# Optimization experiments

Hardware: AMD Instinct MI355X
Metric: run time of the kernel (lower is better)

The kernel has to match this reference:

```python
import jax, jax.numpy as jnp
import numpy as np

NUM_CAPSULE = 10
DIM_CAPSULE = 16
NUM_ROUTING = 3
EPS = 1e-7  # tf.keras.backend.epsilon()


def squash(v, axis=-1):
    s2 = jnp.sum(jnp.square(v), axis=axis, keepdims=True)
    scale = s2 / (1.0 + s2) / jnp.sqrt(s2 + EPS)
    return scale * v


def setup_inputs() -> dict:
    key = jax.random.key(0)
    k1, k2 = jax.random.split(key)
    B, in_dim = 16384, 2048
    inputs = jax.random.normal(k1, (B, in_dim), dtype=jnp.float32)
    # glorot-uniform-ish scale for the kernel
    limit = np.sqrt(6.0 / (in_dim + NUM_CAPSULE * DIM_CAPSULE)).astype(np.float32)
    kernel = jax.random.uniform(k2, (in_dim, NUM_CAPSULE * DIM_CAPSULE),
                                dtype=jnp.float32, minval=-limit, maxval=limit)
    return {"inputs": inputs, "kernel": kernel}


def reference(inputs, kernel):
    B = inputs.shape[0]
    # [B, in_dim] @ [in_dim, nc*dc] -> [B, nc, dc]
    inputs_hat = (inputs @ kernel).reshape(B, NUM_CAPSULE, DIM_CAPSULE)
    b = jnp.zeros((B, NUM_CAPSULE, 1), dtype=inputs.dtype)
    outputs = None
    for _ in range(NUM_ROUTING):
        c = jax.nn.softmax(b, axis=1)                      # [B, nc, 1]
        s = jnp.sum(c * inputs_hat, axis=1, keepdims=True)  # [B, 1, dc]
        outputs = squash(s)                                 # [B, 1, dc]
        # matmul(inputs_hat, outputs, transpose_b=True) -> [B, nc, 1]
        b = b + jnp.einsum('bnd,bd->bn', inputs_hat, outputs[:, 0, :])[:, :, None]
    return outputs[:, 0, :]  # [B, dc]
```

## Files before the change

### kernel.cpp

```cpp
#include <hip/hip_runtime.h>
#include <hip/hip_bf16.h>

typedef unsigned int u32;
typedef unsigned short u16;
typedef __attribute__((ext_vector_type(8))) __bf16 bf16x8;
typedef __attribute__((ext_vector_type(4))) float f32x4;

#define N_CAP 10
#define D_CAP 16
#define NN 160
#define KK 2048
#define BM 64
#define BK 32
#define NSTEPS (KK / BK)
#define THREADS 640
#define LDST 40
#define AS_TILE (BM * LDST)
#define HAT_STRIDE 164
#define SMEM_BYTES (BM * HAT_STRIDE * 4)

__device__ __forceinline__ u32 pack_hi(float f0, float f1) {
  u32 u0 = __builtin_bit_cast(u32, f0), u1 = __builtin_bit_cast(u32, f1);
  return (u0 >> 16) | (u1 & 0xFFFF0000u);
}
__device__ __forceinline__ float hi_part(float f) {
  u32 u = __builtin_bit_cast(u32, f) & 0xFFFF0000u;
  return __builtin_bit_cast(float, u);
}
union U4B8 { uint4 u; bf16x8 b; };

__global__ __launch_bounds__(THREADS, 3) void capsule_fused(
    const float* __restrict__ X, const float* __restrict__ W, float* __restrict__ out) {
  __shared__ __align__(16) char smem[SMEM_BYTES];
  u16* As_hi = (u16*)smem;
  u16* As_lo = As_hi + AS_TILE;
  float* hat = (float*)smem;

  const int t = threadIdx.x;
  const int rbase = blockIdx.x * BM;
  const int lane = t & 63;
  const int w = t >> 6;
  const int wip = (w >= 5) ? 1 : 0;
  const int wjp = w - 5 * wip;
  const int l15 = lane & 15;
  const int q = lane >> 4;

  const int ar = t >> 2;
  const int ak = (t & 3) * 8;
  const float* gA = X + (size_t)(rbase + ar) * KK + ak;

  const float* gB = W + (q * 8) * NN + 32 * wjp + l15;

  f32x4 acc00 = {0.f,0.f,0.f,0.f}, acc01 = {0.f,0.f,0.f,0.f};
  f32x4 acc10 = {0.f,0.f,0.f,0.f}, acc11 = {0.f,0.f,0.f,0.f};

  float4 pa0A, pa1A, pa0B, pa1B;
  if (t < 256) {
    pa0A = *(const float4*)(gA);            pa1A = *(const float4*)(gA + 4);
    pa0B = *(const float4*)(gA + BK);       pa1B = *(const float4*)(gA + BK + 4);
  }
  float buA[16], buB[16];
#pragma unroll
  for (int j = 0; j < 8; ++j) { buA[j] = gB[j * NN]; buA[8 + j] = gB[16 + j * NN]; }

#define STEP(S, PA0, PA1, BU, BNXT)                                              \
  {                                                                              \
    __syncthreads();                            \
    if (t < 256) {                                                               \
      uint4 hi, lo;                                                              \
      hi.x = pack_hi(PA0.x, PA0.y); hi.y = pack_hi(PA0.z, PA0.w);                \
      hi.z = pack_hi(PA1.x, PA1.y); hi.w = pack_hi(PA1.z, PA1.w);                \
      float l0 = PA0.x - hi_part(PA0.x), l1 = PA0.y - hi_part(PA0.y);            \
      float l2 = PA0.z - hi_part(PA0.z), l3 = PA0.w - hi_part(PA0.w);            \
      float l4 = PA1.x - hi_part(PA1.x), l5 = PA1.y - hi_part(PA1.y);            \
      float l6 = PA1.z - hi_part(PA1.z), l7 = PA1.w - hi_part(PA1.w);            \
      lo.x = pack_hi(l0, l1); lo.y = pack_hi(l2, l3);                            \
      lo.z = pack_hi(l4, l5); lo.w = pack_hi(l6, l7);                            \
      *(uint4*)(As_hi + ar * LDST + ak) = hi;                                    \
      *(uint4*)(As_lo + ar * LDST + ak) = lo;                                    \
    }                                                                            \
    __syncthreads();                                             \
    if (t < 256 && (S) + 2 < NSTEPS) {                                           \
      PA0 = *(const float4*)(gA + ((S) + 2) * BK);                               \
      PA1 = *(const float4*)(gA + ((S) + 2) * BK + 4);                           \
    }                                                                            \
    if ((S) + 1 < NSTEPS) {                                                      \
      const float* b = gB + ((S) + 1) * (BK * NN);                               \
      _Pragma("unroll")                                                          \
      for (int j = 0; j < 8; ++j) { BNXT[j] = b[j * NN]; BNXT[8 + j] = b[16 + j * NN]; } \
    }                                                                            \
    U4B8 bh0, bl0, bh1, bl1;                                                     \
    bh0.u.x = pack_hi(BU[0], BU[1]);  bh0.u.y = pack_hi(BU[2], BU[3]);           \
    bh0.u.z = pack_hi(BU[4], BU[5]);  bh0.u.w = pack_hi(BU[6], BU[7]);           \
    bh1.u.x = pack_hi(BU[8], BU[9]);  bh1.u.y = pack_hi(BU[10], BU[11]);         \
    bh1.u.z = pack_hi(BU[12], BU[13]); bh1.u.w = pack_hi(BU[14], BU[15]);        \
    float lb[16];                                                                \
    _Pragma("unroll")                                                            \
    for (int j = 0; j < 16; ++j) lb[j] = BU[j] - hi_part(BU[j]);                 \
    bl0.u.x = pack_hi(lb[0], lb[1]);  bl0.u.y = pack_hi(lb[2], lb[3]);           \
    bl0.u.z = pack_hi(lb[4], lb[5]);  bl0.u.w = pack_hi(lb[6], lb[7]);           \
    bl1.u.x = pack_hi(lb[8], lb[9]);  bl1.u.y = pack_hi(lb[10], lb[11]);         \
    bl1.u.z = pack_hi(lb[12], lb[13]); bl1.u.w = pack_hi(lb[14], lb[15]);        \
    bf16x8 ah0 = *(const bf16x8*)(As_hi + (32 * wip + l15) * LDST + q * 8);      \
    bf16x8 ah1 = *(const bf16x8*)(As_hi + (32 * wip + 16 + l15) * LDST + q * 8); \
    bf16x8 al0 = *(const bf16x8*)(As_lo + (32 * wip + l15) * LDST + q * 8);      \
    bf16x8 al1 = *(const bf16x8*)(As_lo + (32 * wip + 16 + l15) * LDST + q * 8); \
    acc00 = __builtin_amdgcn_mfma_f32_16x16x32_bf16(ah0, bh0.b, acc00, 0, 0, 0); \
    acc00 = __builtin_amdgcn_mfma_f32_16x16x32_bf16(ah0, bl0.b, acc00, 0, 0, 0); \
    acc00 = __builtin_amdgcn_mfma_f32_16x16x32_bf16(al0, bh0.b, acc00, 0, 0, 0); \
    acc01 = __builtin_amdgcn_mfma_f32_16x16x32_bf16(ah0, bh1.b, acc01, 0, 0, 0); \
    acc01 = __builtin_amdgcn_mfma_f32_16x16x32_bf16(ah0, bl1.b, acc01, 0, 0, 0); \
    acc01 = __builtin_amdgcn_mfma_f32_16x16x32_bf16(al0, bh1.b, acc01, 0, 0, 0); \
    acc10 = __builtin_amdgcn_mfma_f32_16x16x32_bf16(ah1, bh0.b, acc10, 0, 0, 0); \
    acc10 = __builtin_amdgcn_mfma_f32_16x16x32_bf16(ah1, bl0.b, acc10, 0, 0, 0); \
    acc10 = __builtin_amdgcn_mfma_f32_16x16x32_bf16(al1, bh0.b, acc10, 0, 0, 0); \
    acc11 = __builtin_amdgcn_mfma_f32_16x16x32_bf16(ah1, bh1.b, acc11, 0, 0, 0); \
    acc11 = __builtin_amdgcn_mfma_f32_16x16x32_bf16(ah1, bl1.b, acc11, 0, 0, 0); \
    acc11 = __builtin_amdgcn_mfma_f32_16x16x32_bf16(al1, bh1.b, acc11, 0, 0, 0); \
  }

  for (int s = 0; s < NSTEPS; s += 2) {
    STEP(s,     pa0A, pa1A, buA, buB)
    STEP(s + 1, pa0B, pa1B, buB, buA)
  }
#undef STEP

  __syncthreads();
#pragma unroll
  for (int r = 0; r < 4; ++r) {
    const int rowb = 32 * wip + 4 * q + r;
    const int colb = 32 * wjp + l15;
    hat[rowb * HAT_STRIDE + colb]             = acc00[r];
    hat[rowb * HAT_STRIDE + colb + 16]        = acc01[r];
    hat[(rowb + 16) * HAT_STRIDE + colb]      = acc10[r];
    hat[(rowb + 16) * HAT_STRIDE + colb + 16] = acc11[r];
  }
  __syncthreads();

  if (t < BM) {
    const int r = t;
    float bb[N_CAP];
#pragma unroll
    for (int n = 0; n < N_CAP; ++n) bb[n] = 0.f;
    float v[D_CAP];
#pragma unroll
    for (int it = 0; it < 3; ++it) {
      float mx = bb[0];
#pragma unroll
      for (int n = 1; n < N_CAP; ++n) mx = fmaxf(mx, bb[n]);
      float c[N_CAP], se = 0.f;
#pragma unroll
      for (int n = 0; n < N_CAP; ++n) { c[n] = __expf(bb[n] - mx); se += c[n]; }
      const float inv = 1.f / se;
      float sd[D_CAP], s2 = 0.f;
#pragma unroll
      for (int d = 0; d < D_CAP; ++d) {
        float x = 0.f;
#pragma unroll
        for (int n = 0; n < N_CAP; ++n) x += c[n] * hat[r * HAT_STRIDE + n * D_CAP + d];
        x *= inv;
        sd[d] = x;
        s2 += x * x;
      }
      const float scale = s2 / ((1.f + s2) * sqrtf(s2 + 1e-7f));
#pragma unroll
      for (int d = 0; d < D_CAP; ++d) v[d] = scale * sd[d];
      if (it < 2) {
#pragma unroll
        for (int n = 0; n < N_CAP; ++n) {
          float dd = 0.f;
#pragma unroll
          for (int d = 0; d < D_CAP; ++d) dd += hat[r * HAT_STRIDE + n * D_CAP + d] * v[d];
          bb[n] += dd;
        }
      }
    }
#pragma unroll
    for (int d = 0; d < D_CAP; ++d)
      out[(size_t)(rbase + r) * D_CAP + d] = v[d];
  }
}

extern "C" void kernel_launch(void* const* d_in, const int* in_sizes, int n_in,
                              void* d_out, int out_size, void* d_ws, size_t ws_size,
                              hipStream_t stream) {
  const float* X = (const float*)d_in[0];
  const float* W = (const float*)d_in[1];
  if (n_in >= 2 && in_sizes[0] == KK * NN) {
    X = (const float*)d_in[1];
    W = (const float*)d_in[0];
  }
  capsule_fused<<<16384 / BM, THREADS, 0, stream>>>(X, W, (float*)d_out);
}
```

Before: 243.5 us.

## Pre-split weights into bf16 hi/lo fragments and restructure GEMM tiling with double-buffered LDS

Adds a small pre-pass kernel that splits W into bf16 hi and lo parts, stored in an MFMA-fragment-friendly layout in the workspace. The main kernel then loads B fragments directly as bf16x8 vectors instead of doing per-step fp32 loads and conversions. It also moves to 32-row blocks with 320 threads and BK=64, and double-buffers the A tile in LDS so there is one barrier per step instead of two. The cost is an extra kernel launch and a pass over W each call, plus more, smaller blocks. The old kernel is kept as a fallback when the workspace is too small.

```diff
diff --git a/kernel.cpp b/kernel.cpp
--- a/kernel.cpp
+++ b/kernel.cpp
@@ -10,6 +10,197 @@
 #define D_CAP 16
 #define NN 160
 #define KK 2048
+
+__device__ __forceinline__ u32 pack_hi(float f0, float f1) {
+  u32 u0 = __builtin_bit_cast(u32, f0), u1 = __builtin_bit_cast(u32, f1);
+  return (u0 >> 16) | (u1 & 0xFFFF0000u);
+}
+__device__ __forceinline__ float hi_part(float f) {
+  u32 u = __builtin_bit_cast(u32, f) & 0xFFFF0000u;
+  return __builtin_bit_cast(float, u);
+}
+union U4B8 { uint4 u; bf16x8 b; };
+
+__global__ void split_w(const float* __restrict__ W, u16* __restrict__ Whi,
+                        u16* __restrict__ Wlo) {
+  const int tid = blockIdx.x * 256 + threadIdx.x;
+  const int k = tid / NN, n = tid - k * NN;
+  const float f = W[tid];
+  const u32 u = __builtin_bit_cast(u32, f);
+  const float lo = f - hi_part(f);
+  const int dst = ((k >> 3) * NN + n) * 8 + (k & 7);
+  Whi[dst] = (u16)(u >> 16);
+  Wlo[dst] = (u16)(__builtin_bit_cast(u32, lo) >> 16);
+}
+
+#define BM2 32
+#define BK2 64
+#define NST2 (KK / BK2)
+#define THR2 320
+#define LDST2 72
+#define ATILE2 2304
+#define BUFU16 4608
+#define SMEM2 20992
+
+__global__ __launch_bounds__(THR2, 3) void capsule_main(
+    const float* __restrict__ X, const u16* __restrict__ Whi,
+    const u16* __restrict__ Wlo, float* __restrict__ out) {
+  __shared__ __align__(16) char smem[SMEM2];
+  u16* As = (u16*)smem;
+  float* hat = (float*)smem;
+
+  const int t = threadIdx.x;
+  const int rbase = blockIdx.x * BM2;
+  const int lane = t & 63;
+  const int w = t >> 6;
+  const int l15 = lane & 15;
+  const int q = lane >> 4;
+
+  const int ar = t >> 3;
+  const int ak = (t & 7) * 8;
+  const float* gA = X + (size_t)(rbase + ar) * KK + ak;
+  const int wA = ar * LDST2 + ak;
+
+  const int gB0 = (q * NN + 32 * w + l15) * 8;
+
+  f32x4 acc00 = {0,0,0,0}, acc01 = {0,0,0,0}, acc10 = {0,0,0,0}, acc11 = {0,0,0,0};
+
+  float4 paA0, paA1, paB0, paB1;
+  bf16x8 BAh[2][2], BAl[2][2], BBh[2][2], BBl[2][2];
+
+  if (t < 256) {
+    paA0 = *(const float4*)(gA);            paA1 = *(const float4*)(gA + 4);
+    paB0 = *(const float4*)(gA + BK2);      paB1 = *(const float4*)(gA + BK2 + 4);
+  }
+#pragma unroll
+  for (int h = 0; h < 2; ++h)
+#pragma unroll
+    for (int i = 0; i < 2; ++i) {
+      BAh[h][i] = *(const bf16x8*)(Whi + gB0 + h * 5120 + i * 128);
+      BAl[h][i] = *(const bf16x8*)(Wlo + gB0 + h * 5120 + i * 128);
+    }
+  if (t < 256) {
+    uint4 hi, lo;
+    hi.x = pack_hi(paA0.x, paA0.y); hi.y = pack_hi(paA0.z, paA0.w);
+    hi.z = pack_hi(paA1.x, paA1.y); hi.w = pack_hi(paA1.z, paA1.w);
+    lo.x = pack_hi(paA0.x - hi_part(paA0.x), paA0.y - hi_part(paA0.y));
+    lo.y = pack_hi(paA0.z - hi_part(paA0.z), paA0.w - hi_part(paA0.w));
+    lo.z = pack_hi(paA1.x - hi_part(paA1.x), paA1.y - hi_part(paA1.y));
+    lo.w = pack_hi(paA1.z - hi_part(paA1.z), paA1.w - hi_part(paA1.w));
+    *(uint4*)(As + wA) = hi;
+    *(uint4*)(As + ATILE2 + wA) = lo;
+  }
+  __syncthreads();
+
+#define STEP2(S, LA0, LA1, SA0, SA1, BH, BL, BHN, BLN)                          \
+  {                                                                             \
+    if ((S) + 1 < NST2) {                                                       \
+      const int bo = gB0 + ((S) + 1) * 10240;                                   \
+      _Pragma("unroll") for (int h = 0; h < 2; ++h)                             \
+      _Pragma("unroll") for (int i = 0; i < 2; ++i) {                           \
+        BHN[h][i] = *(const bf16x8*)(Whi + bo + h * 5120 + i * 128);            \
+        BLN[h][i] = *(const bf16x8*)(Wlo + bo + h * 5120 + i * 128);            \
+      }                                                                         \
+    }                                                                           \
+    if (t < 256 && (S) + 2 < NST2) {                                            \
+      LA0 = *(const float4*)(gA + ((S) + 2) * BK2);                             \
+      LA1 = *(const float4*)(gA + ((S) + 2) * BK2 + 4);                         \
+    }                                                                           \
+    const u16* ab = As + ((S) & 1) * BUFU16;                                    \
+    _Pragma("unroll") for (int h = 0; h < 2; ++h) {                             \
+      bf16x8 ah0 = *(const bf16x8*)(ab + l15 * LDST2 + h * 32 + q * 8);         \
+      bf16x8 ah1 = *(const bf16x8*)(ab + (16 + l15) * LDST2 + h * 32 + q * 8);  \
+      bf16x8 al0 = *(const bf16x8*)(ab + ATILE2 + l15 * LDST2 + h * 32 + q * 8);\
+      bf16x8 al1 = *(const bf16x8*)(ab + ATILE2 + (16 + l15) * LDST2 + h * 32 + q * 8); \
+      acc00 = __builtin_amdgcn_mfma_f32_16x16x32_bf16(ah0, BH[h][0], acc00, 0, 0, 0); \
+      acc00 = __builtin_amdgcn_mfma_f32_16x16x32_bf16(ah0, BL[h][0], acc00, 0, 0, 0); \
+      acc00 = __builtin_amdgcn_mfma_f32_16x16x32_bf16(al0, BH[h][0], acc00, 0, 0, 0); \
+      acc01 = __builtin_amdgcn_mfma_f32_16x16x32_bf16(ah0, BH[h][1], acc01, 0, 0, 0); \
+      acc01 = __builtin_amdgcn_mfma_f32_16x16x32_bf16(ah0, BL[h][1], acc01, 0, 0, 0); \
+      acc01 = __builtin_amdgcn_mfma_f32_16x16x32_bf16(al0, BH[h][1], acc01, 0, 0, 0); \
+      acc10 = __builtin_amdgcn_mfma_f32_16x16x32_bf16(ah1, BH[h][0], acc10, 0, 0, 0); \
+      acc10 = __builtin_amdgcn_mfma_f32_16x16x32_bf16(ah1, BL[h][0], acc10, 0, 0, 0); \
+      acc10 = __builtin_amdgcn_mfma_f32_16x16x32_bf16(al1, BH[h][0], acc10, 0, 0, 0); \
+      acc11 = __builtin_amdgcn_mfma_f32_16x16x32_bf16(ah1, BH[h][1], acc11, 0, 0, 0); \
+      acc11 = __builtin_amdgcn_mfma_f32_16x16x32_bf16(ah1, BL[h][1], acc11, 0, 0, 0); \
+      acc11 = __builtin_amdgcn_mfma_f32_16x16x32_bf16(al1, BH[h][1], acc11, 0, 0, 0); \
+    }                                                                           \
+    if (t < 256 && (S) + 1 < NST2) {                                            \
+      u16* wb = As + (((S) + 1) & 1) * BUFU16;                                  \
+      uint4 hi, lo;                                                             \
+      hi.x = pack_hi(SA0.x, SA0.y); hi.y = pack_hi(SA0.z, SA0.w);               \
+      hi.z = pack_hi(SA1.x, SA1.y); hi.w = pack_hi(SA1.z, SA1.w);               \
+      lo.x = pack_hi(SA0.x - hi_part(SA0.x), SA0.y - hi_part(SA0.y));           \
+      lo.y = pack_hi(SA0.z - hi_part(SA0.z), SA0.w - hi_part(SA0.w));           \
+      lo.z = pack_hi(SA1.x - hi_part(SA1.x), SA1.y - hi_part(SA1.y));           \
+      lo.w = pack_hi(SA1.z - hi_part(SA1.z), SA1.w - hi_part(SA1.w));           \
+      *(uint4*)(wb + wA) = hi;                                                  \
+      *(uint4*)(wb + ATILE2 + wA) = lo;                                         \
+    }                                                                           \
+    __syncthreads();                                                            \
+  }
+
+  for (int s = 0; s < NST2; s += 2) {
+    STEP2(s,     paA0, paA1, paB0, paB1, BAh, BAl, BBh, BBl)
+    STEP2(s + 1, paB0, paB1, paA0, paA1, BBh, BBl, BAh, BAl)
+  }
+#undef STEP2
+
+#pragma unroll
+  for (int r = 0; r < 4; ++r) {
+    const int rowb = 4 * q + r;
+    const int colb = 32 * w + l15;
+    hat[rowb * 164 + colb]             = acc00[r];
+    hat[rowb * 164 + colb + 16]        = acc01[r];
+    hat[(rowb + 16) * 164 + colb]      = acc10[r];
+    hat[(rowb + 16) * 164 + colb + 16] = acc11[r];
+  }
+  __syncthreads();
+
+  if (t < BM2) {
+    const int r = t;
+    float bb[N_CAP];
+#pragma unroll
+    for (int n = 0; n < N_CAP; ++n) bb[n] = 0.f;
+    float v[D_CAP];
+#pragma unroll
+    for (int it = 0; it < 3; ++it) {
+      float mx = bb[0];
+#pragma unroll
+      for (int n = 1; n < N_CAP; ++n) mx = fmaxf(mx, bb[n]);
+      float c[N_CAP], se = 0.f;
+#pragma unroll
+      for (int n = 0; n < N_CAP; ++n) { c[n] = __expf(bb[n] - mx); se += c[n]; }
+      const float inv = 1.f / se;
+      float sd[D_CAP], s2 = 0.f;
+#pragma unroll
+      for (int d = 0; d < D_CAP; ++d) {
+        float x = 0.f;
+#pragma unroll
+        for (int n = 0; n < N_CAP; ++n) x += c[n] * hat[r * 164 + n * D_CAP + d];
+        x *= inv;
+        sd[d] = x;
+        s2 += x * x;
+      }
+      const float scale = s2 / ((1.f + s2) * sqrtf(s2 + 1e-7f));
+#pragma unroll
+      for (int d = 0; d < D_CAP; ++d) v[d] = scale * sd[d];
+      if (it < 2) {
+#pragma unroll
+        for (int n = 0; n < N_CAP; ++n) {
+          float dd = 0.f;
+#pragma unroll
+          for (int d = 0; d < D_CAP; ++d) dd += hat[r * 164 + n * D_CAP + d] * v[d];
+          bb[n] += dd;
+        }
+      }
+    }
+#pragma unroll
+    for (int d = 0; d < D_CAP; ++d)
+      out[(size_t)(rbase + r) * D_CAP + d] = v[d];
+  }
+}
+
 #define BM 64
 #define BK 32
 #define NSTEPS (KK / BK)
@@ -19,23 +210,12 @@
 #define HAT_STRIDE 164
 #define SMEM_BYTES (BM * HAT_STRIDE * 4)
 
-__device__ __forceinline__ u32 pack_hi(float f0, float f1) {
-  u32 u0 = __builtin_bit_cast(u32, f0), u1 = __builtin_bit_cast(u32, f1);
-  return (u0 >> 16) | (u1 & 0xFFFF0000u);
-}
-__device__ __forceinline__ float hi_part(float f) {
-  u32 u = __builtin_bit_cast(u32, f) & 0xFFFF0000u;
-  return __builtin_bit_cast(float, u);
-}
-union U4B8 { uint4 u; bf16x8 b; };
-
-__global__ __launch_bounds__(THREADS, 3) void capsule_fused(
+__global__ __launch_bounds__(THREADS, 3) void capsule_fb(
     const float* __restrict__ X, const float* __restrict__ W, float* __restrict__ out) {
   __shared__ __align__(16) char smem[SMEM_BYTES];
   u16* As_hi = (u16*)smem;
   u16* As_lo = As_hi + AS_TILE;
   float* hat = (float*)smem;
-
   const int t = threadIdx.x;
   const int rbase = blockIdx.x * BM;
   const int lane = t & 63;
@@ -44,42 +224,34 @@
   const int wjp = w - 5 * wip;
   const int l15 = lane & 15;
   const int q = lane >> 4;
-
   const int ar = t >> 2;
   const int ak = (t & 3) * 8;
   const float* gA = X + (size_t)(rbase + ar) * KK + ak;
-
   const float* gB = W + (q * 8) * NN + 32 * wjp + l15;
-
-  f32x4 acc00 = {0.f,0.f,0.f,0.f}, acc01 = {0.f,0.f,0.f,0.f};
-  f32x4 acc10 = {0.f,0.f,0.f,0.f}, acc11 = {0.f,0.f,0.f,0.f};
-
+  f32x4 acc00 = {0,0,0,0}, acc01 = {0,0,0,0}, acc10 = {0,0,0,0}, acc11 = {0,0,0,0};
   float4 pa0A, pa1A, pa0B, pa1B;
   if (t < 256) {
-    pa0A = *(const float4*)(gA);            pa1A = *(const float4*)(gA + 4);
-    pa0B = *(const float4*)(gA + BK);       pa1B = *(const float4*)(gA + BK + 4);
+    pa0A = *(const float4*)(gA);        pa1A = *(const float4*)(gA + 4);
+    pa0B = *(const float4*)(gA + BK);   pa1B = *(const float4*)(gA + BK + 4);
   }
   float buA[16], buB[16];
 #pragma unroll
   for (int j = 0; j < 8; ++j) { buA[j] = gB[j * NN]; buA[8 + j] = gB[16 + j * NN]; }
-
 #define STEP(S, PA0, PA1, BU, BNXT)                                              \
   {                                                                              \
-    __syncthreads();                            \
+    __syncthreads();                                                             \
     if (t < 256) {                                                               \
       uint4 hi, lo;                                                              \
       hi.x = pack_hi(PA0.x, PA0.y); hi.y = pack_hi(PA0.z, PA0.w);                \
       hi.z = pack_hi(PA1.x, PA1.y); hi.w = pack_hi(PA1.z, PA1.w);                \
-      float l0 = PA0.x - hi_part(PA0.x), l1 = PA0.y - hi_part(PA0.y);            \
-      float l2 = PA0.z - hi_part(PA0.z), l3 = PA0.w - hi_part(PA0.w);            \
-      float l4 = PA1.x - hi_part(PA1.x), l5 = PA1.y - hi_part(PA1.y);            \
-      float l6 = PA1.z - hi_part(PA1.z), l7 = PA1.w - hi_part(PA1.w);            \
-      lo.x = pack_hi(l0, l1); lo.y = pack_hi(l2, l3);                            \
-      lo.z = pack_hi(l4, l5); lo.w = pack_hi(l6, l7);                            \
+      lo.x = pack_hi(PA0.x - hi_part(PA0.x), PA0.y - hi_part(PA0.y));            \
+      lo.y = pack_hi(PA0.z - hi_part(PA0.z), PA0.w - hi_part(PA0.w));            \
+      lo.z = pack_hi(PA1.x - hi_part(PA1.x), PA1.y - hi_part(PA1.y));            \
+      lo.w = pack_hi(PA1.z - hi_part(PA1.z), PA1.w - hi_part(PA1.w));            \
       *(uint4*)(As_hi + ar * LDST + ak) = hi;                                    \
       *(uint4*)(As_lo + ar * LDST + ak) = lo;                                    \
     }                                                                            \
-    __syncthreads();                                             \
+    __syncthreads();                                                             \
     if (t < 256 && (S) + 2 < NSTEPS) {                                           \
       PA0 = *(const float4*)(gA + ((S) + 2) * BK);                               \
       PA1 = *(const float4*)(gA + ((S) + 2) * BK + 4);                           \
@@ -118,13 +290,11 @@
     acc11 = __builtin_amdgcn_mfma_f32_16x16x32_bf16(ah1, bl1.b, acc11, 0, 0, 0); \
     acc11 = __builtin_amdgcn_mfma_f32_16x16x32_bf16(al1, bh1.b, acc11, 0, 0, 0); \
   }
-
   for (int s = 0; s < NSTEPS; s += 2) {
     STEP(s,     pa0A, pa1A, buA, buB)
     STEP(s + 1, pa0B, pa1B, buB, buA)
   }
 #undef STEP
-
   __syncthreads();
 #pragma unroll
   for (int r = 0; r < 4; ++r) {
@@ -136,7 +306,6 @@
     hat[(rowb + 16) * HAT_STRIDE + colb + 16] = acc11[r];
   }
   __syncthreads();
-
   if (t < BM) {
     const int r = t;
     float bb[N_CAP];
@@ -190,5 +359,13 @@
     X = (const float*)d_in[1];
     W = (const float*)d_in[0];
   }
-  capsule_fused<<<16384 / BM, THREADS, 0, stream>>>(X, W, (float*)d_out);
-}
+  const size_t need = (size_t)2 * KK * NN * sizeof(u16);
+  if (ws_size >= need) {
+    u16* Whi = (u16*)d_ws;
+    u16* Wlo = Whi + (size_t)KK * NN;
+    split_w<<<(KK * NN) / 256, 256, 0, stream>>>(W, Whi, Wlo);
+    capsule_main<<<16384 / BM2, THR2, 0, stream>>>(X, Whi, Wlo, (float*)d_out);
+  } else {
+    capsule_fb<<<16384 / BM, THREADS, 0, stream>>>(X, W, (float*)d_out);
+  }
+}
```

After: 244.2 us. No clear change (+0.3%).

## Split into weight pre-split, split-K GEMM with LDS-staged W, and routing reduction

Applied to the files above, without the earlier changes.

Adds a three-kernel path used when the workspace is large enough. The first kernel converts W once into hi/lo bf16 halves in an MFMA-friendly layout. The second runs a split-K (two halves) GEMM over 128-row tiles, streaming the pre-split W into LDS with global_load_lds double buffering and feeding A directly from registers. The third sums the partial products and runs the dynamic routing. This removes the per-block repeated W conversion and LDS staging of A, and raises per-block reuse and parallelism. In exchange it writes and re-reads a large partial buffer and adds two extra launches; the old fused kernel stays as a fallback.

```diff
diff --git a/kernel.cpp b/kernel.cpp
--- a/kernel.cpp
+++ b/kernel.cpp
@@ -10,6 +10,208 @@
 #define D_CAP 16
 #define NN 160
 #define KK 2048
+
+__device__ __forceinline__ u32 pack_hi(float f0, float f1) {
+  u32 u0 = __builtin_bit_cast(u32, f0), u1 = __builtin_bit_cast(u32, f1);
+  return (u0 >> 16) | (u1 & 0xFFFF0000u);
+}
+__device__ __forceinline__ float hi_part(float f) {
+  u32 u = __builtin_bit_cast(u32, f) & 0xFFFF0000u;
+  return __builtin_bit_cast(float, u);
+}
+
+__device__ __forceinline__ void gl_lds16(const void* g, void* l) {
+  __builtin_amdgcn_global_load_lds((const __attribute__((address_space(1))) void*)g,
+                                   (__attribute__((address_space(3))) void*)l, 16, 0, 0);
+}
+
+__device__ __forceinline__ void split8(const float4& A, const float4& B,
+                                       bf16x8& h, bf16x8& l) {
+  union { u32 u[4]; bf16x8 b; } H, L;
+  H.u[0] = pack_hi(A.x, A.y); H.u[1] = pack_hi(A.z, A.w);
+  H.u[2] = pack_hi(B.x, B.y); H.u[3] = pack_hi(B.z, B.w);
+  L.u[0] = pack_hi(A.x - hi_part(A.x), A.y - hi_part(A.y));
+  L.u[1] = pack_hi(A.z - hi_part(A.z), A.w - hi_part(A.w));
+  L.u[2] = pack_hi(B.x - hi_part(B.x), B.y - hi_part(B.y));
+  L.u[3] = pack_hi(B.z - hi_part(B.z), B.w - hi_part(B.w));
+  h = H.b; l = L.b;
+}
+
+__global__ void split_w(const float* __restrict__ W, u16* __restrict__ Whi,
+                        u16* __restrict__ Wlo) {
+  const int tid = blockIdx.x * 256 + threadIdx.x;
+  const int k = tid / NN, n = tid - k * NN;
+  const float f = W[tid];
+  const u32 u = __builtin_bit_cast(u32, f);
+  const float lo = f - hi_part(f);
+  const int dst = ((k >> 3) * NN + n) * 8 + (k & 7);
+  Whi[dst] = (u16)(u >> 16);
+  Wlo[dst] = (u16)(__builtin_bit_cast(u32, lo) >> 16);
+}
+
+#define BMm 128
+#define KH 1024
+#define BKm 32
+#define NSTm (KH / BKm)
+#define THRm 640
+#define PSTRIDE (BMm * NN)
+#define P_OFF_BYTES (2 * KK * NN * 2)
+#define WS_NEED ((size_t)P_OFF_BYTES + (size_t)256 * PSTRIDE * 4)
+
+__global__ __launch_bounds__(THRm) void gemm_splitk(
+    const float* __restrict__ X, const u16* __restrict__ Whi,
+    const u16* __restrict__ Wlo, float* __restrict__ P) {
+  __shared__ __align__(16) char smem[40960];
+  const int t = threadIdx.x;
+  const int b = blockIdx.x;
+  const int rt = b & 127, kh = b >> 7;
+  const int rbase = rt * BMm;
+  const int lane = t & 63;
+  const int w = t >> 6;
+  const int wg = (w >= 5) ? 1 : 0;
+  const int wc = w - 5 * wg;
+  const int l15 = lane & 15, q = lane >> 4;
+
+  const u16* WhiK = Whi + (size_t)(kh * 128) * 1280 + t * 8;
+  const u16* WloK = Wlo + (size_t)(kh * 128) * 1280 + t * 8;
+
+  const float* gA[4];
+#pragma unroll
+  for (int m = 0; m < 4; ++m)
+    gA[m] = X + (size_t)(rbase + 64 * wg + 16 * m + l15) * KK + kh * KH + q * 8;
+
+  const int bofs0 = (q * 160 + 32 * wc + l15) * 16;
+  const int bofs1 = (q * 160 + 32 * wc + 16 + l15) * 16;
+
+  f32x4 acc[4][2];
+#pragma unroll
+  for (int m = 0; m < 4; ++m)
+#pragma unroll
+    for (int i = 0; i < 2; ++i) acc[m][i] = (f32x4){0.f, 0.f, 0.f, 0.f};
+
+  float4 aA[4][2], aB[4][2];
+
+  gl_lds16(WhiK, smem + t * 16);
+  gl_lds16(WloK, smem + 10240 + t * 16);
+#pragma unroll
+  for (int m = 0; m < 4; ++m) {
+    aA[m][0] = *(const float4*)(gA[m]);
+    aA[m][1] = *(const float4*)(gA[m] + 4);
+    aB[m][0] = *(const float4*)(gA[m] + BKm);
+    aB[m][1] = *(const float4*)(gA[m] + BKm + 4);
+  }
+  __syncthreads();
+
+#define HALFSTEP(S, AREG)                                                        \
+  {                                                                              \
+    if ((S) + 1 < NSTm) {                 \
+      const u16* sh = WhiK + ((S) + 1) * 5120;                                   \
+      const u16* sl = WloK + ((S) + 1) * 5120;                                   \
+      char* dst = smem + (((S) + 1) & 1) * 20480;                                \
+      gl_lds16(sh, dst + t * 16);                                                \
+      gl_lds16(sl, dst + 10240 + t * 16);                                        \
+    }                                                                            \
+    bf16x8 ah[4], al[4];                                                         \
+    _Pragma("unroll") for (int m = 0; m < 4; ++m)                                \
+      split8(AREG[m][0], AREG[m][1], ah[m], al[m]);                              \
+    if ((S) + 2 < NSTm) {                  \
+      _Pragma("unroll") for (int m = 0; m < 4; ++m) {                            \
+        AREG[m][0] = *(const float4*)(gA[m] + ((S) + 2) * BKm);                  \
+        AREG[m][1] = *(const float4*)(gA[m] + ((S) + 2) * BKm + 4);              \
+      }                                                                          \
+    }                                                                            \
+    const char* bb = smem + ((S) & 1) * 20480;                                   \
+    bf16x8 bh0 = *(const bf16x8*)(bb + bofs0);                                   \
+    bf16x8 bh1 = *(const bf16x8*)(bb + bofs1);                                   \
+    bf16x8 bl0 = *(const bf16x8*)(bb + 10240 + bofs0);                           \
+    bf16x8 bl1 = *(const bf16x8*)(bb + 10240 + bofs1);                           \
+    _Pragma("unroll") for (int m = 0; m < 4; ++m) {                              \
+      acc[m][0] = __builtin_amdgcn_mfma_f32_16x16x32_bf16(ah[m], bh0, acc[m][0], 0, 0, 0); \
+      acc[m][0] = __builtin_amdgcn_mfma_f32_16x16x32_bf16(ah[m], bl0, acc[m][0], 0, 0, 0); \
+      acc[m][0] = __builtin_amdgcn_mfma_f32_16x16x32_bf16(al[m], bh0, acc[m][0], 0, 0, 0); \
+      acc[m][1] = __builtin_amdgcn_mfma_f32_16x16x32_bf16(ah[m], bh1, acc[m][1], 0, 0, 0); \
+      acc[m][1] = __builtin_amdgcn_mfma_f32_16x16x32_bf16(ah[m], bl1, acc[m][1], 0, 0, 0); \
+      acc[m][1] = __builtin_amdgcn_mfma_f32_16x16x32_bf16(al[m], bh1, acc[m][1], 0, 0, 0); \
+    }                                                                            \
+    __syncthreads();             \
+  }
+
+#pragma unroll 1
+  for (int s = 0; s < NSTm; s += 2) {
+    HALFSTEP(s, aA)
+    HALFSTEP(s + 1, aB)
+  }
+#undef HALFSTEP
+
+  float* Pb = P + (size_t)b * PSTRIDE;
+#pragma unroll
+  for (int m = 0; m < 4; ++m)
+#pragma unroll
+    for (int i = 0; i < 2; ++i)
+#pragma unroll
+      for (int r = 0; r < 4; ++r) {
+        const int rr = 64 * wg + 16 * m + q * 4 + r;
+        const int n = 32 * wc + 16 * i + l15;
+        Pb[rr * NN + n] = acc[m][i][r];
+      }
+}
+
+__global__ __launch_bounds__(64) void reduce_route(
+    const float* __restrict__ P, float* __restrict__ out) {
+  __shared__ float hat[64 * 164];
+  const int blk = blockIdx.x;
+  const int t = threadIdx.x;
+  const int r0 = blk * 64;
+  const int rt = r0 >> 7;
+  for (int i = t; i < 64 * NN; i += 64) {
+    const int r = i / NN, n = i - r * NN;
+    const int rr = (r0 + r) & 127;
+    hat[r * 164 + n] = P[(size_t)rt * PSTRIDE + rr * NN + n] +
+                       P[(size_t)(128 + rt) * PSTRIDE + rr * NN + n];
+  }
+  __syncthreads();
+  const int r = t;
+  float bb[N_CAP];
+#pragma unroll
+  for (int n = 0; n < N_CAP; ++n) bb[n] = 0.f;
+  float v[D_CAP];
+#pragma unroll
+  for (int it = 0; it < 3; ++it) {
+    float mx = bb[0];
+#pragma unroll
+    for (int n = 1; n < N_CAP; ++n) mx = fmaxf(mx, bb[n]);
+    float c[N_CAP], se = 0.f;
+#pragma unroll
+    for (int n = 0; n < N_CAP; ++n) { c[n] = __expf(bb[n] - mx); se += c[n]; }
+    const float inv = 1.f / se;
+    float sd[D_CAP], s2 = 0.f;
+#pragma unroll
+    for (int d = 0; d < D_CAP; ++d) {
+      float x = 0.f;
+#pragma unroll
+      for (int n = 0; n < N_CAP; ++n) x += c[n] * hat[r * 164 + n * D_CAP + d];
+      x *= inv;
+      sd[d] = x;
+      s2 += x * x;
+    }
+    const float scale = s2 / ((1.f + s2) * sqrtf(s2 + 1e-7f));
+#pragma unroll
+    for (int d = 0; d < D_CAP; ++d) v[d] = scale * sd[d];
+    if (it < 2) {
+#pragma unroll
+      for (int n = 0; n < N_CAP; ++n) {
+        float dd = 0.f;
+#pragma unroll
+        for (int d = 0; d < D_CAP; ++d) dd += hat[r * 164 + n * D_CAP + d] * v[d];
+        bb[n] += dd;
+      }
+    }
+  }
+#pragma unroll
+  for (int d = 0; d < D_CAP; ++d)
+    out[(size_t)(r0 + r) * D_CAP + d] = v[d];
+}
+
 #define BM 64
 #define BK 32
 #define NSTEPS (KK / BK)
@@ -18,24 +220,14 @@
 #define AS_TILE (BM * LDST)
 #define HAT_STRIDE 164
 #define SMEM_BYTES (BM * HAT_STRIDE * 4)
-
-__device__ __forceinline__ u32 pack_hi(float f0, float f1) {
-  u32 u0 = __builtin_bit_cast(u32, f0), u1 = __builtin_bit_cast(u32, f1);
-  return (u0 >> 16) | (u1 & 0xFFFF0000u);
-}
-__device__ __forceinline__ float hi_part(float f) {
-  u32 u = __builtin_bit_cast(u32, f) & 0xFFFF0000u;
-  return __builtin_bit_cast(float, u);
-}
 union U4B8 { uint4 u; bf16x8 b; };
 
-__global__ __launch_bounds__(THREADS, 3) void capsule_fused(
+__global__ __launch_bounds__(THREADS, 3) void capsule_fb(
     const float* __restrict__ X, const float* __restrict__ W, float* __restrict__ out) {
   __shared__ __align__(16) char smem[SMEM_BYTES];
   u16* As_hi = (u16*)smem;
   u16* As_lo = As_hi + AS_TILE;
   float* hat = (float*)smem;
-
   const int t = threadIdx.x;
   const int rbase = blockIdx.x * BM;
   const int lane = t & 63;
@@ -44,50 +236,42 @@
   const int wjp = w - 5 * wip;
   const int l15 = lane & 15;
   const int q = lane >> 4;
-
   const int ar = t >> 2;
   const int ak = (t & 3) * 8;
   const float* gA = X + (size_t)(rbase + ar) * KK + ak;
-
   const float* gB = W + (q * 8) * NN + 32 * wjp + l15;
-
-  f32x4 acc00 = {0.f,0.f,0.f,0.f}, acc01 = {0.f,0.f,0.f,0.f};
-  f32x4 acc10 = {0.f,0.f,0.f,0.f}, acc11 = {0.f,0.f,0.f,0.f};
-
+  f32x4 acc00 = {0,0,0,0}, acc01 = {0,0,0,0}, acc10 = {0,0,0,0}, acc11 = {0,0,0,0};
   float4 pa0A, pa1A, pa0B, pa1B;
   if (t < 256) {
-    pa0A = *(const float4*)(gA);            pa1A = *(const float4*)(gA + 4);
-    pa0B = *(const float4*)(gA + BK);       pa1B = *(const float4*)(gA + BK + 4);
+    pa0A = *(const float4*)(gA);        pa1A = *(const float4*)(gA + 4);
+    pa0B = *(const float4*)(gA + BK);   pa1B = *(const float4*)(gA + BK + 4);
   }
   float buA[16], buB[16];
 #pragma unroll
   for (int j = 0; j < 8; ++j) { buA[j] = gB[j * NN]; buA[8 + j] = gB[16 + j * NN]; }
-
 #define STEP(S, PA0, PA1, BU, BNXT)                                              \
   {                                                                              \
-    __syncthreads();                            \
+    __syncthreads();                                                             \
     if (t < 256) {                                                               \
       uint4 hi, lo;                                                              \
       hi.x = pack_hi(PA0.x, PA0.y); hi.y = pack_hi(PA0.z, PA0.w);                \
       hi.z = pack_hi(PA1.x, PA1.y); hi.w = pack_hi(PA1.z, PA1.w);                \
-      float l0 = PA0.x - hi_part(PA0.x), l1 = PA0.y - hi_part(PA0.y);            \
-      float l2 = PA0.z - hi_part(PA0.z), l3 = PA0.w - hi_part(PA0.w);            \
-      float l4 = PA1.x - hi_part(PA1.x), l5 = PA1.y - hi_part(PA1.y);            \
-      float l6 = PA1.z - hi_part(PA1.z), l7 = PA1.w - hi_part(PA1.w);            \
-      lo.x = pack_hi(l0, l1); lo.y = pack_hi(l2, l3);                            \
-      lo.z = pack_hi(l4, l5); lo.w = pack_hi(l6, l7);                            \
+      lo.x = pack_hi(PA0.x - hi_part(PA0.x), PA0.y - hi_part(PA0.y));            \
+      lo.y = pack_hi(PA0.z - hi_part(PA0.z), PA0.w - hi_part(PA0.w));            \
+      lo.z = pack_hi(PA1.x - hi_part(PA1.x), PA1.y - hi_part(PA1.y));            \
+      lo.w = pack_hi(PA1.z - hi_part(PA1.z), PA1.w - hi_part(PA1.w));            \
       *(uint4*)(As_hi + ar * LDST + ak) = hi;                                    \
       *(uint4*)(As_lo + ar * LDST + ak) = lo;                                    \
     }                                                                            \
-    __syncthreads();                                             \
+    __syncthreads();                                                             \
     if (t < 256 && (S) + 2 < NSTEPS) {                                           \
       PA0 = *(const float4*)(gA + ((S) + 2) * BK);                               \
       PA1 = *(const float4*)(gA + ((S) + 2) * BK + 4);                           \
     }                                                                            \
     if ((S) + 1 < NSTEPS) {                                                      \
-      const float* b = gB + ((S) + 1) * (BK * NN);                               \
+      const float* bsrc = gB + ((S) + 1) * (BK * NN);                            \
       _Pragma("unroll")                                                          \
-      for (int j = 0; j < 8; ++j) { BNXT[j] = b[j * NN]; BNXT[8 + j] = b[16 + j * NN]; } \
+      for (int j = 0; j < 8; ++j) { BNXT[j] = bsrc[j * NN]; BNXT[8 + j] = bsrc[16 + j * NN]; } \
     }                                                                            \
     U4B8 bh0, bl0, bh1, bl1;                                                     \
     bh0.u.x = pack_hi(BU[0], BU[1]);  bh0.u.y = pack_hi(BU[2], BU[3]);           \
@@ -118,13 +302,11 @@
     acc11 = __builtin_amdgcn_mfma_f32_16x16x32_bf16(ah1, bl1.b, acc11, 0, 0, 0); \
     acc11 = __builtin_amdgcn_mfma_f32_16x16x32_bf16(al1, bh1.b, acc11, 0, 0, 0); \
   }
-
   for (int s = 0; s < NSTEPS; s += 2) {
     STEP(s,     pa0A, pa1A, buA, buB)
     STEP(s + 1, pa0B, pa1B, buB, buA)
   }
 #undef STEP
-
   __syncthreads();
 #pragma unroll
   for (int r = 0; r < 4; ++r) {
@@ -136,7 +318,6 @@
     hat[(rowb + 16) * HAT_STRIDE + colb + 16] = acc11[r];
   }
   __syncthreads();
-
   if (t < BM) {
     const int r = t;
     float bb[N_CAP];
@@ -190,5 +371,14 @@
     X = (const float*)d_in[1];
     W = (const float*)d_in[0];
   }
-  capsule_fused<<<16384 / BM, THREADS, 0, stream>>>(X, W, (float*)d_out);
-}
+  if (ws_size >= WS_NEED) {
+    u16* Whi = (u16*)d_ws;
+    u16* Wlo = Whi + (size_t)KK * NN;
+    float* P = (float*)((char*)d_ws + P_OFF_BYTES);
+    split_w<<<(KK * NN) / 256, 256, 0, stream>>>(W, Whi, Wlo);
+    gemm_splitk<<<256, THRm, 0, stream>>>(X, Whi, Wlo, P);
+    reduce_route<<<256, 64, 0, stream>>>(P, (float*)d_out);
+  } else {
+    capsule_fb<<<16384 / BM, THREADS, 0, stream>>>(X, W, (float*)d_out);
+  }
+}
```

Result: slower. 277.4 us (+13.9%).
